# Optimization experiments

Measured on AMD Instinct MI355X. Metric: run time of the kernel, lower is better.

The kernel has to match this reference:

```python
import jax, jax.numpy as jnp
import numpy as np

N_NODES = 100000
SAMPLES = 16


def setup_inputs() -> dict:
    key = jax.random.key(0)
    ks = jax.random.split(key, 9)
    x = jax.random.normal(ks[0], (N_NODES, 128), dtype=jnp.float32)
    neigh_idx = jax.random.randint(ks[1], (N_NODES, SAMPLES), 0, N_NODES)
    batch = jax.random.randint(ks[2], (8192,), 0, N_NODES)
    W1 = jax.random.normal(ks[3], (256, 128), dtype=jnp.float32) * 0.05
    b1 = jax.random.normal(ks[4], (128,), dtype=jnp.float32) * 0.05
    W2 = jax.random.normal(ks[5], (256, 128), dtype=jnp.float32) * 0.05
    b2 = jax.random.normal(ks[6], (128,), dtype=jnp.float32) * 0.05
    Wout = jax.random.normal(ks[7], (128, 64), dtype=jnp.float32) * 0.05
    bout = jax.random.normal(ks[8], (64,), dtype=jnp.float32) * 0.05
    return {"x": x, "neigh_idx": neigh_idx, "batch": batch,
            "W1": W1, "b1": b1, "W2": W2, "b2": b2,
            "Wout": Wout, "bout": bout}


def _sage_layer(h, neigh_idx, W, b):
    # h: [N, d]; gather sampled neighbors -> [N, S, d]; max-aggregate; concat-linear
    neigh = h[neigh_idx]                     # irregular gather, memory-bound core
    agg = jnp.max(neigh, axis=1)             # MaxAggregation over samples
    feats = jnp.concatenate([h, agg], axis=-1)  # [N, 2d]
    return feats @ W + b


def reference(x, neigh_idx, batch, W1, b1, W2, b2, Wout, bout):
    # layer 1: relu(Linear(concat(x, max_neigh(x))))
    h1 = jax.nn.relu(_sage_layer(x, neigh_idx, W1, b1))
    # layer 2 (== n_layers): Linear output (no relu) fed straight into proj_out
    h2 = _sage_layer(h1, neigh_idx, W2, b2)
    out = h2 @ Wout + bout                   # proj_out (Dropout is eval identity)
    return out[batch]
```

## Files before the change

kernel.cpp:

```cpp
#include <hip/hip_runtime.h>
#include <cmath>
#include <cstdint>

#define N_NODES 100000
#define SAMPLES 16
#define DIM 128
#define NBATCH 8192

#define FSTR 264
#define H2STR 132

typedef _Float16 half8 __attribute__((ext_vector_type(8)));
typedef float floatx4 __attribute__((ext_vector_type(4)));

__device__ __forceinline__ half8 h8max(half8 a, half8 b) {
    half8 r;
#pragma unroll
    for (int i = 0; i < 8; ++i) r[i] = (a[i] > b[i]) ? a[i] : b[i];
    return r;
}

__global__ void zero_flags(int* __restrict__ flags) {
    int i = blockIdx.x * blockDim.x + threadIdx.x;
    if (i < N_NODES) flags[i] = 0;
}

__global__ void mark_flags(const int* __restrict__ batch,
                           const int* __restrict__ nidx,
                           int* __restrict__ flags) {
    int j = blockIdx.x * blockDim.x + threadIdx.x;
    if (j >= NBATCH) return;
    int b = batch[j];
    flags[b] = 1;
    const int* row = nidx + (size_t)b * SAMPLES;
#pragma unroll
    for (int s = 0; s < SAMPLES; ++s) flags[row[s]] = 1;
}

__global__ __launch_bounds__(256) void cvt_x(const float* __restrict__ x,
                                             _Float16* __restrict__ xh) {
    const int tid = blockIdx.x * blockDim.x + threadIdx.x;
    const size_t base = (size_t)tid * 8;
    if (base >= (size_t)N_NODES * DIM) return;
    const float4* xp = (const float4*)(x + base);
    const float4 a = xp[0], b = xp[1];
    half8 v;
    v[0] = (_Float16)a.x; v[1] = (_Float16)a.y;
    v[2] = (_Float16)a.z; v[3] = (_Float16)a.w;
    v[4] = (_Float16)b.x; v[5] = (_Float16)b.y;
    v[6] = (_Float16)b.z; v[7] = (_Float16)b.w;
    *(half8*)(xh + base) = v;
}

__global__ __launch_bounds__(256) void swizzle_w(const float* __restrict__ W1,
                                                 const float* __restrict__ W2,
                                                 _Float16* __restrict__ W1sw,
                                                 _Float16* __restrict__ W2sw) {
    const int tid = blockIdx.x * blockDim.x + threadIdx.x;
    const int which = tid >> 12;
    const int r = tid & 4095;
    const int kb = r >> 9, nb = (r >> 6) & 7, lane = r & 63;
    const int q = lane >> 4, c = lane & 15;
    const float* W = which ? W2 : W1;
    _Float16* O = which ? W2sw : W1sw;
    const int k0 = kb * 32 + q * 8;
    const int n = nb * 16 + c;
    half8 v;
#pragma unroll
    for (int j = 0; j < 8; ++j) v[j] = (_Float16)W[(size_t)(k0 + j) * DIM + n];
    *(half8*)(O + (size_t)r * 8) = v;
}

__global__ __launch_bounds__(256) void layer1_kernel(
    const _Float16* __restrict__ xh,
    const int* __restrict__ nidx,
    const _Float16* __restrict__ W1sw,
    const float* __restrict__ b1,
    const int* __restrict__ flags,
    _Float16* __restrict__ h1h) {
    const int wave = threadIdx.x >> 6;
    const int lane = threadIdx.x & 63;
    const int q = lane >> 4;
    const int c = lane & 15;
    const int w0 = blockIdx.x * 64 + wave * 16;

    __shared__ __align__(16) _Float16 feats[4][16 * FSTR];
    _Float16* fw = feats[wave];

#pragma unroll
    for (int ng = 0; ng < 4; ++ng) {
        const int m = ng * 4 + q;
        const int i = w0 + m;
        const bool valid = (i < N_NODES) && flags[i];
        if (valid) {
            const half8 s = *(const half8*)(xh + (size_t)i * DIM + c * 8);
            *(half8*)(fw + m * FSTR + c * 8) = s;
            half8 mx;
#pragma unroll
            for (int e = 0; e < 8; ++e) mx[e] = (_Float16)(-60000.f);
            const int* row = nidx + (size_t)i * SAMPLES;
#pragma unroll
            for (int s2 = 0; s2 < SAMPLES; ++s2) {
                const int nb = row[s2];
                const half8 v = *(const half8*)(xh + (size_t)nb * DIM + c * 8);
                mx = h8max(mx, v);
            }
            *(half8*)(fw + m * FSTR + DIM + c * 8) = mx;
        }
    }
    __syncthreads();

    floatx4 acc[8];
#pragma unroll
    for (int nb = 0; nb < 8; ++nb) acc[nb] = (floatx4){0.f, 0.f, 0.f, 0.f};

#pragma unroll
    for (int kb = 0; kb < 8; ++kb) {
        const half8 a = *(const half8*)(fw + c * FSTR + kb * 32 + q * 8);
#pragma unroll
        for (int nb = 0; nb < 8; ++nb) {
            const half8 b = *(const half8*)(W1sw + (size_t)((kb * 8 + nb) * 64 + lane) * 8);
            acc[nb] = __builtin_amdgcn_mfma_f32_16x16x32_f16(a, b, acc[nb], 0, 0, 0);
        }
    }

    int fl[4];
#pragma unroll
    for (int r = 0; r < 4; ++r) {
        const int i = w0 + q * 4 + r;
        fl[r] = (i < N_NODES) && flags[i];
    }
#pragma unroll
    for (int nb = 0; nb < 8; ++nb) {
        const int n = nb * 16 + c;
        const float bias = b1[n];
#pragma unroll
        for (int r = 0; r < 4; ++r) {
            if (!fl[r]) continue;
            const int i = w0 + q * 4 + r;
            const float v = fmaxf(acc[nb][r] + bias, 0.f);
            h1h[(size_t)i * DIM + n] = (_Float16)v;
        }
    }
}

__global__ __launch_bounds__(64) void layer2_kernel(
    const _Float16* __restrict__ h1h,
    const int* __restrict__ nidx,
    const int* __restrict__ batch,
    const _Float16* __restrict__ W2sw,
    const float* __restrict__ b2,
    const float* __restrict__ Wout,
    const float* __restrict__ bout,
    float* __restrict__ out) {
    const int lane = threadIdx.x;
    const int q = lane >> 4, c = lane & 15;
    const int w0 = blockIdx.x * 16;

    __shared__ __align__(16) _Float16 feats[16 * FSTR];
    __shared__ __align__(16) float h2s[16 * H2STR];

#pragma unroll
    for (int ng = 0; ng < 4; ++ng) {
        const int m = ng * 4 + q;
        const int node = batch[w0 + m];
        const half8 s = *(const half8*)(h1h + (size_t)node * DIM + c * 8);
        *(half8*)(feats + m * FSTR + c * 8) = s;
        half8 mx;
#pragma unroll
        for (int e = 0; e < 8; ++e) mx[e] = (_Float16)(-60000.f);
        const int* row = nidx + (size_t)node * SAMPLES;
#pragma unroll
        for (int s2 = 0; s2 < SAMPLES; ++s2) {
            const int nb = row[s2];
            const half8 v = *(const half8*)(h1h + (size_t)nb * DIM + c * 8);
            mx = h8max(mx, v);
        }
        *(half8*)(feats + m * FSTR + DIM + c * 8) = mx;
    }
    __syncthreads();

    floatx4 acc[8];
#pragma unroll
    for (int nb = 0; nb < 8; ++nb) acc[nb] = (floatx4){0.f, 0.f, 0.f, 0.f};

#pragma unroll
    for (int kb = 0; kb < 8; ++kb) {
        const half8 a = *(const half8*)(feats + c * FSTR + kb * 32 + q * 8);
#pragma unroll
        for (int nb = 0; nb < 8; ++nb) {
            const half8 b = *(const half8*)(W2sw + (size_t)((kb * 8 + nb) * 64 + lane) * 8);
            acc[nb] = __builtin_amdgcn_mfma_f32_16x16x32_f16(a, b, acc[nb], 0, 0, 0);
        }
    }

#pragma unroll
    for (int nb = 0; nb < 8; ++nb) {
        const float bias = b2[nb * 16 + c];
#pragma unroll
        for (int r = 0; r < 4; ++r)
            h2s[(q * 4 + r) * H2STR + nb * 16 + c] = acc[nb][r] + bias;
    }
    __syncthreads();

    float accs[16];
    const float bo = bout[lane];
#pragma unroll
    for (int m = 0; m < 16; ++m) accs[m] = bo;
    for (int k4 = 0; k4 < DIM; k4 += 4) {
        float wv[4];
#pragma unroll
        for (int j = 0; j < 4; ++j) wv[j] = Wout[(size_t)(k4 + j) * 64 + lane];
#pragma unroll
        for (int m = 0; m < 16; ++m) {
            const float4 f = *(const float4*)&h2s[m * H2STR + k4];
            accs[m] += f.x * wv[0] + f.y * wv[1] + f.z * wv[2] + f.w * wv[3];
        }
    }
#pragma unroll
    for (int m = 0; m < 16; ++m)
        out[(size_t)(w0 + m) * 64 + lane] = accs[m];
}

extern "C" void kernel_launch(void* const* d_in, const int* in_sizes, int n_in,
                              void* d_out, int out_size, void* d_ws, size_t ws_size,
                              hipStream_t stream) {
    const float* x    = (const float*)d_in[0];
    const int* nidx   = (const int*)d_in[1];
    const int* batch  = (const int*)d_in[2];
    const float* W1   = (const float*)d_in[3];
    const float* b1   = (const float*)d_in[4];
    const float* W2   = (const float*)d_in[5];
    const float* b2   = (const float*)d_in[6];
    const float* Wout = (const float*)d_in[7];
    const float* bout = (const float*)d_in[8];
    float* out        = (float*)d_out;

    int* flags      = (int*)d_ws;
    _Float16* W1sw  = (_Float16*)((char*)d_ws + 409600);
    _Float16* W2sw  = (_Float16*)((char*)d_ws + 475136);
    _Float16* xh    = (_Float16*)((char*)d_ws + 540672);
    _Float16* h1h   = (_Float16*)((char*)d_ws + 26140672);

    zero_flags<<<(N_NODES + 255) / 256, 256, 0, stream>>>(flags);
    mark_flags<<<(NBATCH + 255) / 256, 256, 0, stream>>>(batch, nidx, flags);
    cvt_x<<<(N_NODES * DIM / 8 + 255) / 256, 256, 0, stream>>>(x, xh);
    swizzle_w<<<32, 256, 0, stream>>>(W1, W2, W1sw, W2sw);
    layer1_kernel<<<(N_NODES + 63) / 64, 256, 0, stream>>>(xh, nidx, W1sw, b1, flags, h1h);
    layer2_kernel<<<NBATCH / 16, 64, 0, stream>>>(h1h, nidx, batch, W2sw, b2, Wout, bout, out);
}
```

Baseline: 197.9 us.

## Fuse setup kernels, prefetch neighbor indices, tree-reduce gathers, widen layer2 blocks

Merges x conversion, flag zeroing and weight swizzling into one setup kernel to cut launch overhead. In layer1, neighbor index rows are loaded as int4 and prefetched one group ahead, and all 16 neighbor rows are issued before a tree max-reduction, which raises memory-level parallelism. Layer2 moves to 4 waves per block, each wave gathering 4 nodes and computing 2 MFMA column tiles plus a quarter of the output projection, so per-wave serial work drops. The layer1 epilogue now contains a dead loop and re-reads flags from global memory, which adds a little redundant work.

```diff
diff --git a/kernel.cpp b/kernel.cpp
--- a/kernel.cpp
+++ b/kernel.cpp
@@ -20,14 +20,48 @@
     return r;
 }
 
-__global__ void zero_flags(int* __restrict__ flags) {
-    int i = blockIdx.x * blockDim.x + threadIdx.x;
-    if (i < N_NODES) flags[i] = 0;
-}
-
-__global__ void mark_flags(const int* __restrict__ batch,
-                           const int* __restrict__ nidx,
-                           int* __restrict__ flags) {
+__global__ __launch_bounds__(256) void setup_kernel(
+    const float* __restrict__ x,
+    const float* __restrict__ W1,
+    const float* __restrict__ W2,
+    int* __restrict__ flags,
+    _Float16* __restrict__ xh,
+    _Float16* __restrict__ W1sw,
+    _Float16* __restrict__ W2sw) {
+    const int bid = blockIdx.x;
+    if (bid < 6250) {
+        const size_t base = ((size_t)bid * 256 + threadIdx.x) * 8;
+        const float4* xp = (const float4*)(x + base);
+        const float4 a = xp[0], b = xp[1];
+        half8 v;
+        v[0] = (_Float16)a.x; v[1] = (_Float16)a.y;
+        v[2] = (_Float16)a.z; v[3] = (_Float16)a.w;
+        v[4] = (_Float16)b.x; v[5] = (_Float16)b.y;
+        v[6] = (_Float16)b.z; v[7] = (_Float16)b.w;
+        *(half8*)(xh + base) = v;
+    } else if (bid < 6641) {
+        const int i = (bid - 6250) * 256 + threadIdx.x;
+        if (i < N_NODES) flags[i] = 0;
+    } else {
+        const int tid = (bid - 6641) * 256 + threadIdx.x;
+        const int which = tid >> 12;
+        const int r = tid & 4095;
+        const int kb = r >> 9, nb = (r >> 6) & 7, lane = r & 63;
+        const int q = lane >> 4, c = lane & 15;
+        const float* W = which ? W2 : W1;
+        _Float16* O = which ? W2sw : W1sw;
+        const int k0 = kb * 32 + q * 8;
+        const int n = nb * 16 + c;
+        half8 v;
+#pragma unroll
+        for (int j = 0; j < 8; ++j) v[j] = (_Float16)W[(size_t)(k0 + j) * DIM + n];
+        *(half8*)(O + (size_t)r * 8) = v;
+    }
+}
+
+__global__ __launch_bounds__(256) void mark_flags(const int* __restrict__ batch,
+                                                  const int* __restrict__ nidx,
+                                                  int* __restrict__ flags) {
     int j = blockIdx.x * blockDim.x + threadIdx.x;
     if (j >= NBATCH) return;
     int b = batch[j];
@@ -35,40 +69,6 @@
     const int* row = nidx + (size_t)b * SAMPLES;
 #pragma unroll
     for (int s = 0; s < SAMPLES; ++s) flags[row[s]] = 1;
-}
-
-__global__ __launch_bounds__(256) void cvt_x(const float* __restrict__ x,
-                                             _Float16* __restrict__ xh) {
-    const int tid = blockIdx.x * blockDim.x + threadIdx.x;
-    const size_t base = (size_t)tid * 8;
-    if (base >= (size_t)N_NODES * DIM) return;
-    const float4* xp = (const float4*)(x + base);
-    const float4 a = xp[0], b = xp[1];
-    half8 v;
-    v[0] = (_Float16)a.x; v[1] = (_Float16)a.y;
-    v[2] = (_Float16)a.z; v[3] = (_Float16)a.w;
-    v[4] = (_Float16)b.x; v[5] = (_Float16)b.y;
-    v[6] = (_Float16)b.z; v[7] = (_Float16)b.w;
-    *(half8*)(xh + base) = v;
-}
-
-__global__ __launch_bounds__(256) void swizzle_w(const float* __restrict__ W1,
-                                                 const float* __restrict__ W2,
-                                                 _Float16* __restrict__ W1sw,
-                                                 _Float16* __restrict__ W2sw) {
-    const int tid = blockIdx.x * blockDim.x + threadIdx.x;
-    const int which = tid >> 12;
-    const int r = tid & 4095;
-    const int kb = r >> 9, nb = (r >> 6) & 7, lane = r & 63;
-    const int q = lane >> 4, c = lane & 15;
-    const float* W = which ? W2 : W1;
-    _Float16* O = which ? W2sw : W1sw;
-    const int k0 = kb * 32 + q * 8;
-    const int n = nb * 16 + c;
-    half8 v;
-#pragma unroll
-    for (int j = 0; j < 8; ++j) v[j] = (_Float16)W[(size_t)(k0 + j) * DIM + n];
-    *(half8*)(O + (size_t)r * 8) = v;
 }
 
 __global__ __launch_bounds__(256) void layer1_kernel(
@@ -87,33 +87,63 @@
     __shared__ __align__(16) _Float16 feats[4][16 * FSTR];
     _Float16* fw = feats[wave];
 
+    int fl[4];
 #pragma unroll
     for (int ng = 0; ng < 4; ++ng) {
-        const int m = ng * 4 + q;
-        const int i = w0 + m;
-        const bool valid = (i < N_NODES) && flags[i];
-        if (valid) {
-            const half8 s = *(const half8*)(xh + (size_t)i * DIM + c * 8);
-            *(half8*)(fw + m * FSTR + c * 8) = s;
-            half8 mx;
-#pragma unroll
-            for (int e = 0; e < 8; ++e) mx[e] = (_Float16)(-60000.f);
-            const int* row = nidx + (size_t)i * SAMPLES;
-#pragma unroll
-            for (int s2 = 0; s2 < SAMPLES; ++s2) {
-                const int nb = row[s2];
-                const half8 v = *(const half8*)(xh + (size_t)nb * DIM + c * 8);
-                mx = h8max(mx, v);
-            }
-            *(half8*)(fw + m * FSTR + DIM + c * 8) = mx;
-        }
+        const int i = w0 + ng * 4 + q;
+        fl[ng] = (i < N_NODES) ? flags[i] : 0;
+    }
+    int4 cur0, cur1, cur2, cur3;
+    {
+        int i = w0 + q; if (i >= N_NODES) i = N_NODES - 1;
+        const int4* rp = (const int4*)(nidx + (size_t)i * SAMPLES);
+        cur0 = rp[0]; cur1 = rp[1]; cur2 = rp[2]; cur3 = rp[3];
+    }
+    const size_t co = (size_t)c * 8;
+#pragma unroll
+    for (int ng = 0; ng < 4; ++ng) {
+        int4 nx0, nx1, nx2, nx3;
+        if (ng < 3) {
+            int i = w0 + (ng + 1) * 4 + q; if (i >= N_NODES) i = N_NODES - 1;
+            const int4* rp = (const int4*)(nidx + (size_t)i * SAMPLES);
+            nx0 = rp[0]; nx1 = rp[1]; nx2 = rp[2]; nx3 = rp[3];
+        }
+        if (fl[ng]) {
+            const int m = ng * 4 + q;
+            const int i = w0 + m;
+            const half8 self = *(const half8*)(xh + (size_t)i * DIM + co);
+            *(half8*)(fw + m * FSTR + c * 8) = self;
+            half8 v[16];
+            v[0]  = *(const half8*)(xh + (size_t)cur0.x * DIM + co);
+            v[1]  = *(const half8*)(xh + (size_t)cur0.y * DIM + co);
+            v[2]  = *(const half8*)(xh + (size_t)cur0.z * DIM + co);
+            v[3]  = *(const half8*)(xh + (size_t)cur0.w * DIM + co);
+            v[4]  = *(const half8*)(xh + (size_t)cur1.x * DIM + co);
+            v[5]  = *(const half8*)(xh + (size_t)cur1.y * DIM + co);
+            v[6]  = *(const half8*)(xh + (size_t)cur1.z * DIM + co);
+            v[7]  = *(const half8*)(xh + (size_t)cur1.w * DIM + co);
+            v[8]  = *(const half8*)(xh + (size_t)cur2.x * DIM + co);
+            v[9]  = *(const half8*)(xh + (size_t)cur2.y * DIM + co);
+            v[10] = *(const half8*)(xh + (size_t)cur2.z * DIM + co);
+            v[11] = *(const half8*)(xh + (size_t)cur2.w * DIM + co);
+            v[12] = *(const half8*)(xh + (size_t)cur3.x * DIM + co);
+            v[13] = *(const half8*)(xh + (size_t)cur3.y * DIM + co);
+            v[14] = *(const half8*)(xh + (size_t)cur3.z * DIM + co);
+            v[15] = *(const half8*)(xh + (size_t)cur3.w * DIM + co);
+#pragma unroll
+            for (int s = 0; s < 8; ++s) v[s] = h8max(v[s], v[s + 8]);
+#pragma unroll
+            for (int s = 0; s < 4; ++s) v[s] = h8max(v[s], v[s + 4]);
+            v[0] = h8max(h8max(v[0], v[1]), h8max(v[2], v[3]));
+            *(half8*)(fw + m * FSTR + DIM + c * 8) = v[0];
+        }
+        if (ng < 3) { cur0 = nx0; cur1 = nx1; cur2 = nx2; cur3 = nx3; }
     }
     __syncthreads();
 
     floatx4 acc[8];
 #pragma unroll
     for (int nb = 0; nb < 8; ++nb) acc[nb] = (floatx4){0.f, 0.f, 0.f, 0.f};
-
 #pragma unroll
     for (int kb = 0; kb < 8; ++kb) {
         const half8 a = *(const half8*)(fw + c * FSTR + kb * 32 + q * 8);
@@ -123,28 +153,31 @@
             acc[nb] = __builtin_amdgcn_mfma_f32_16x16x32_f16(a, b, acc[nb], 0, 0, 0);
         }
     }
-
-    int fl[4];
-#pragma unroll
-    for (int r = 0; r < 4; ++r) {
-        const int i = w0 + q * 4 + r;
-        fl[r] = (i < N_NODES) && flags[i];
-    }
 #pragma unroll
     for (int nb = 0; nb < 8; ++nb) {
         const int n = nb * 16 + c;
         const float bias = b1[n];
 #pragma unroll
         for (int r = 0; r < 4; ++r) {
-            if (!fl[r]) continue;
+            const int m = q * 4 + r;
+            if (!fl[m >> 2]) continue;
+        }
+    }
+#pragma unroll
+    for (int nb = 0; nb < 8; ++nb) {
+        const int n = nb * 16 + c;
+        const float bias = b1[n];
+#pragma unroll
+        for (int r = 0; r < 4; ++r) {
             const int i = w0 + q * 4 + r;
+            if (i >= N_NODES || !flags[i]) continue;
             const float v = fmaxf(acc[nb][r] + bias, 0.f);
             h1h[(size_t)i * DIM + n] = (_Float16)v;
         }
     }
 }
 
-__global__ __launch_bounds__(64) void layer2_kernel(
+__global__ __launch_bounds__(256) void layer2_kernel(
     const _Float16* __restrict__ h1h,
     const int* __restrict__ nidx,
     const int* __restrict__ batch,
@@ -153,73 +186,88 @@
     const float* __restrict__ Wout,
     const float* __restrict__ bout,
     float* __restrict__ out) {
-    const int lane = threadIdx.x;
+    const int wave = threadIdx.x >> 6;
+    const int lane = threadIdx.x & 63;
     const int q = lane >> 4, c = lane & 15;
     const int w0 = blockIdx.x * 16;
 
     __shared__ __align__(16) _Float16 feats[16 * FSTR];
     __shared__ __align__(16) float h2s[16 * H2STR];
 
-#pragma unroll
-    for (int ng = 0; ng < 4; ++ng) {
-        const int m = ng * 4 + q;
+    {
+        const int m = wave * 4 + q;
         const int node = batch[w0 + m];
-        const half8 s = *(const half8*)(h1h + (size_t)node * DIM + c * 8);
-        *(half8*)(feats + m * FSTR + c * 8) = s;
-        half8 mx;
-#pragma unroll
-        for (int e = 0; e < 8; ++e) mx[e] = (_Float16)(-60000.f);
-        const int* row = nidx + (size_t)node * SAMPLES;
-#pragma unroll
-        for (int s2 = 0; s2 < SAMPLES; ++s2) {
-            const int nb = row[s2];
-            const half8 v = *(const half8*)(h1h + (size_t)nb * DIM + c * 8);
-            mx = h8max(mx, v);
-        }
-        *(half8*)(feats + m * FSTR + DIM + c * 8) = mx;
+        const size_t co = (size_t)c * 8;
+        const int4* rp = (const int4*)(nidx + (size_t)node * SAMPLES);
+        const int4 i0 = rp[0], i1 = rp[1], i2 = rp[2], i3 = rp[3];
+        const half8 self = *(const half8*)(h1h + (size_t)node * DIM + co);
+        *(half8*)(feats + m * FSTR + c * 8) = self;
+        half8 v[16];
+        v[0]  = *(const half8*)(h1h + (size_t)i0.x * DIM + co);
+        v[1]  = *(const half8*)(h1h + (size_t)i0.y * DIM + co);
+        v[2]  = *(const half8*)(h1h + (size_t)i0.z * DIM + co);
+        v[3]  = *(const half8*)(h1h + (size_t)i0.w * DIM + co);
+        v[4]  = *(const half8*)(h1h + (size_t)i1.x * DIM + co);
+        v[5]  = *(const half8*)(h1h + (size_t)i1.y * DIM + co);
+        v[6]  = *(const half8*)(h1h + (size_t)i1.z * DIM + co);
+        v[7]  = *(const half8*)(h1h + (size_t)i1.w * DIM + co);
+        v[8]  = *(const half8*)(h1h + (size_t)i2.x * DIM + co);
+        v[9]  = *(const half8*)(h1h + (size_t)i2.y * DIM + co);
+        v[10] = *(const half8*)(h1h + (size_t)i2.z * DIM + co);
+        v[11] = *(const half8*)(h1h + (size_t)i2.w * DIM + co);
+        v[12] = *(const half8*)(h1h + (size_t)i3.x * DIM + co);
+        v[13] = *(const half8*)(h1h + (size_t)i3.y * DIM + co);
+        v[14] = *(const half8*)(h1h + (size_t)i3.z * DIM + co);
+        v[15] = *(const half8*)(h1h + (size_t)i3.w * DIM + co);
+#pragma unroll
+        for (int s = 0; s < 8; ++s) v[s] = h8max(v[s], v[s + 8]);
+#pragma unroll
+        for (int s = 0; s < 4; ++s) v[s] = h8max(v[s], v[s + 4]);
+        v[0] = h8max(h8max(v[0], v[1]), h8max(v[2], v[3]));
+        *(half8*)(feats + m * FSTR + DIM + c * 8) = v[0];
     }
     __syncthreads();
 
-    floatx4 acc[8];
-#pragma unroll
-    for (int nb = 0; nb < 8; ++nb) acc[nb] = (floatx4){0.f, 0.f, 0.f, 0.f};
-
+    const int nb0 = wave * 2;
+    floatx4 acc[2];
+    acc[0] = (floatx4){0.f, 0.f, 0.f, 0.f};
+    acc[1] = (floatx4){0.f, 0.f, 0.f, 0.f};
 #pragma unroll
     for (int kb = 0; kb < 8; ++kb) {
         const half8 a = *(const half8*)(feats + c * FSTR + kb * 32 + q * 8);
 #pragma unroll
-        for (int nb = 0; nb < 8; ++nb) {
-            const half8 b = *(const half8*)(W2sw + (size_t)((kb * 8 + nb) * 64 + lane) * 8);
-            acc[nb] = __builtin_amdgcn_mfma_f32_16x16x32_f16(a, b, acc[nb], 0, 0, 0);
-        }
-    }
-
-#pragma unroll
-    for (int nb = 0; nb < 8; ++nb) {
-        const float bias = b2[nb * 16 + c];
+        for (int j = 0; j < 2; ++j) {
+            const half8 b = *(const half8*)(W2sw + (size_t)((kb * 8 + nb0 + j) * 64 + lane) * 8);
+            acc[j] = __builtin_amdgcn_mfma_f32_16x16x32_f16(a, b, acc[j], 0, 0, 0);
+        }
+    }
+#pragma unroll
+    for (int j = 0; j < 2; ++j) {
+        const int n = (nb0 + j) * 16 + c;
+        const float bias = b2[n];
 #pragma unroll
         for (int r = 0; r < 4; ++r)
-            h2s[(q * 4 + r) * H2STR + nb * 16 + c] = acc[nb][r] + bias;
+            h2s[(q * 4 + r) * H2STR + n] = acc[j][r] + bias;
     }
     __syncthreads();
 
-    float accs[16];
+    float accs[4];
     const float bo = bout[lane];
 #pragma unroll
-    for (int m = 0; m < 16; ++m) accs[m] = bo;
+    for (int r = 0; r < 4; ++r) accs[r] = bo;
     for (int k4 = 0; k4 < DIM; k4 += 4) {
         float wv[4];
 #pragma unroll
         for (int j = 0; j < 4; ++j) wv[j] = Wout[(size_t)(k4 + j) * 64 + lane];
 #pragma unroll
-        for (int m = 0; m < 16; ++m) {
-            const float4 f = *(const float4*)&h2s[m * H2STR + k4];
-            accs[m] += f.x * wv[0] + f.y * wv[1] + f.z * wv[2] + f.w * wv[3];
-        }
-    }
-#pragma unroll
-    for (int m = 0; m < 16; ++m)
-        out[(size_t)(w0 + m) * 64 + lane] = accs[m];
+        for (int r = 0; r < 4; ++r) {
+            const float4 f = *(const float4*)&h2s[(wave * 4 + r) * H2STR + k4];
+            accs[r] += f.x * wv[0] + f.y * wv[1] + f.z * wv[2] + f.w * wv[3];
+        }
+    }
+#pragma unroll
+    for (int r = 0; r < 4; ++r)
+        out[(size_t)(w0 + wave * 4 + r) * 64 + lane] = accs[r];
 }
 
 extern "C" void kernel_launch(void* const* d_in, const int* in_sizes, int n_in,
@@ -242,10 +290,8 @@
     _Float16* xh    = (_Float16*)((char*)d_ws + 540672);
     _Float16* h1h   = (_Float16*)((char*)d_ws + 26140672);
 
-    zero_flags<<<(N_NODES + 255) / 256, 256, 0, stream>>>(flags);
-    mark_flags<<<(NBATCH + 255) / 256, 256, 0, stream>>>(batch, nidx, flags);
-    cvt_x<<<(N_NODES * DIM / 8 + 255) / 256, 256, 0, stream>>>(x, xh);
-    swizzle_w<<<32, 256, 0, stream>>>(W1, W2, W1sw, W2sw);
+    setup_kernel<<<6673, 256, 0, stream>>>(x, W1, W2, flags, xh, W1sw, W2sw);
+    mark_flags<<<32, 256, 0, stream>>>(batch, nidx, flags);
     layer1_kernel<<<(N_NODES + 63) / 64, 256, 0, stream>>>(xh, nidx, W1sw, b1, flags, h1h);
-    layer2_kernel<<<NBATCH / 16, 64, 0, stream>>>(h1h, nidx, batch, W2sw, b2, Wout, bout, out);
-}
+    layer2_kernel<<<NBATCH / 16, 256, 0, stream>>>(h1h, nidx, batch, W2sw, b2, Wout, bout, out);
+}
```

Result: no change. 194.5 us (-1.7%).
